# Kernel tuning notes

Measured on AMD Instinct MI355X. Metric: run time of the kernel, lower is better.

Reference implementation:

```python
import jax, jax.numpy as jnp
import numpy as np

H = 2048      # hidden_dim
DI = 4096     # intermediate_size
N = 128       # state_size
NH = 64       # num_heads
P = 64        # head_dim
K = 4         # conv kernel
CH = 256      # chunk size
L = 4096      # seq len
DT_MIN, DT_MAX = 1e-3, 1e2


def setup_inputs() -> dict:
    key = jax.random.key(0)
    ks = jax.random.split(key, 8)
    conv_dim = DI + 2 * N
    x = jax.random.normal(ks[0], (L, H), jnp.float32)
    W_in = jax.random.normal(ks[1], (DI + 2 * N + NH, H), jnp.float32) / np.sqrt(H)
    conv_w = jax.random.normal(ks[2], (conv_dim, 1, K), jnp.float32) / np.sqrt(K)
    conv_b = jax.random.normal(ks[3], (conv_dim,), jnp.float32) * 0.01
    u = jax.random.uniform(ks[4], (NH,))
    dt = jnp.exp(u * (np.log(0.1) - np.log(0.001)) + np.log(0.001))
    dt = jnp.maximum(dt, 1e-4)
    dt_bias = dt + jnp.log(-jnp.expm1(-dt))   # inverse-softplus init
    A_log = jnp.log(jax.random.uniform(ks[5], (NH,), minval=1.0, maxval=16.0))
    D = jnp.ones((NH,), jnp.float32)
    norm_w = jnp.ones((DI,), jnp.float32)
    W_out = jax.random.normal(ks[6], (H, DI), jnp.float32) / np.sqrt(DI)
    return dict(x=x, W_in=W_in, conv_w=conv_w, conv_b=conv_b, dt_bias=dt_bias,
                A_log=A_log, D=D, norm_w=norm_w, W_out=W_out)


def _causal_decay(a):
    # a: [..., T] per-step log-decays -> exp(segment sum) as lower-tri [..., T, T]
    T = a.shape[-1]
    strict = jnp.tril(jnp.ones((T, T), bool), -1)
    full = jnp.tril(jnp.ones((T, T), bool), 0)
    s = jnp.cumsum(jnp.where(strict, a[..., None], 0.0), axis=-2)
    return jnp.where(full, jnp.exp(s), 0.0)


def reference(x, W_in, conv_w, conv_b, dt_bias, A_log, D, norm_w, W_out):
    conv_dim = DI + 2 * N
    xBCdt = x @ W_in.T                                  # [L, DI+2N+NH]
    xBC, dt = xBCdt[:, :conv_dim], xBCdt[:, conv_dim:]
    # causal depthwise conv1d + SiLU
    z = jax.lax.conv_general_dilated(
        xBC.T[None], conv_w, (1,), [(K - 1, 0)],
        dimension_numbers=('NCH', 'OIH', 'NCH'),
        feature_group_count=conv_dim)[0] + conv_b[:, None]
    xBC = jax.nn.silu(z.T)                              # [L, conv_dim]
    x_ssm = xBC[:, :DI].reshape(L, NH, P)
    Bm = xBC[:, DI:DI + N]                              # [L, N] shared over heads
    Cm = xBC[:, DI + N:]                                # [L, N]
    dt = jnp.clip(jax.nn.softplus(dt + dt_bias), DT_MIN, DT_MAX)  # [L, NH]
    A = -jnp.exp(A_log.astype(jnp.float32))             # [NH]
    dA = dt * A                                         # [L, NH]
    xdt = x_ssm * dt[:, :, None]                        # [L, NH, P]
    nc = L // CH
    xc = xdt.reshape(nc, CH, NH, P)
    Bc = Bm.reshape(nc, CH, N)
    Cc = Cm.reshape(nc, CH, N)
    dAc = dA.reshape(nc, CH, NH)
    A_cs = jnp.cumsum(dAc, axis=1)                      # [c, k, h]
    # intra-chunk (diagonal blocks)
    Lmat = _causal_decay(dAc.transpose(0, 2, 1))        # [c, h, k, k]
    Y_diag = jnp.einsum('ckn,csn,chks,cshp->ckhp', Cc, Bc, Lmat, xc)
    # per-chunk right states
    decay_states = jnp.exp(A_cs[:, -1:, :] - A_cs)      # [c, k, h]
    states = jnp.einsum('ckn,ckh,ckhp->chpn', Bc, decay_states, xc)
    # inter-chunk recurrence (no initial state)
    chunk_sum = A_cs[:, -1, :].T                        # [h, c]
    dec = _causal_decay(jnp.pad(chunk_sum, ((0, 0), (1, 0))))  # [h, c+1, c+1]
    states = jnp.concatenate([jnp.zeros((1, NH, P, N), states.dtype), states], 0)
    new_states = jnp.einsum('hzc,chpn->zhpn', dec, states)      # [c+1, h, p, n]
    prev = new_states[:-1]                              # [c, h, p, n]
    Y_off = jnp.einsum('ckn,chpn,ckh->ckhp', Cc, prev, jnp.exp(A_cs))
    Y = (Y_diag + Y_off).reshape(L, NH, P) + x_ssm * D[None, :, None]
    y = Y.reshape(L, DI)
    # RMSNorm
    var = jnp.mean(jnp.square(y.astype(jnp.float32)), -1, keepdims=True)
    y = (y * jax.lax.rsqrt(var + 1e-6)) * norm_w
    return y @ W_out.T
```

## Files before the change

kernel.cpp:

```cpp
#include <hip/hip_runtime.h>


typedef __bf16 bf16;
typedef __bf16 bf16x8 __attribute__((ext_vector_type(8)));
typedef __bf16 bf16x4 __attribute__((ext_vector_type(4)));
typedef float  f32x4  __attribute__((ext_vector_type(4)));

#define DEV static __device__ __forceinline__

DEV f32x4 mfma16(bf16x8 a, bf16x8 b, f32x4 c) {
  return __builtin_amdgcn_mfma_f32_16x16x32_bf16(a, b, c, 0, 0, 0);
}

DEV void gll16(const bf16* g, bf16* l) {
  __builtin_amdgcn_global_load_lds(
      (const __attribute__((address_space(1))) unsigned int*)g,
      (__attribute__((address_space(3))) unsigned int*)l, 16, 0, 0);
}

#define BAR()   asm volatile("s_barrier" ::: "memory")
#define LGKM0() do { asm volatile("s_waitcnt lgkmcnt(0)" ::: "memory"); \
                     __builtin_amdgcn_sched_barrier(0); } while (0)
#define VMW(n)  asm volatile("s_waitcnt vmcnt(" #n ")" ::: "memory")

template <int K>
__global__ __launch_bounds__(512) void gemm8p_kernel(
    const bf16* __restrict__ A, const bf16* __restrict__ B,
    float* __restrict__ C, int N, int ntN) {
  constexpr int NT = K / 64;
  __shared__ __align__(16) bf16 lds[3 * 24576];
  const int tid = threadIdx.x;
  const int wave = tid >> 6, lane = tid & 63;
  const int lrow = lane & 15;
  const int lkb = (lane >> 4) * 16;
  const int xorv = (lrow & 7) << 4;
  const int bx = blockIdx.x / ntN, by = blockIdx.x % ntN;
  const int row0 = bx * 256, col0 = by * 128;
  const int arow = (wave >> 1) * 64;
  const int brow = (wave & 1) * 64;

  const bf16* gA[4];
  const bf16* gB[2];
#pragma unroll
  for (int r = 0; r < 4; ++r) {
    int P = r * 8192 + tid * 16;
    int L = P ^ (((P >> 7) & 7) << 4);
    gA[r] = A + (size_t)(row0 + (L >> 7)) * K + ((L & 127) >> 1);
  }
#pragma unroll
  for (int r = 0; r < 2; ++r) {
    int P = r * 8192 + tid * 16;
    int L = P ^ (((P >> 7) & 7) << 4);
    gB[r] = B + (size_t)(col0 + (L >> 7)) * K + ((L & 127) >> 1);
  }
  const int ldsW = wave * 512;

  auto rdA = [&](int slB, int m, int ks) -> bf16x8 {
    return *(const bf16x8*)((const char*)lds + slB +
                            (arow + m * 16 + lrow) * 128 +
                            (((ks << 6) | lkb) ^ xorv));
  };
  auto rdB = [&](int slB, int n, int ks) -> bf16x8 {
    return *(const bf16x8*)((const char*)lds + slB + 32768 +
                            (brow + n * 16 + lrow) * 128 +
                            (((ks << 6) | lkb) ^ xorv));
  };
  auto stA01 = [&](int ss) {
    gll16(gA[0], lds + ss * 24576 + 0 * 4096 + ldsW);
    gll16(gA[1], lds + ss * 24576 + 1 * 4096 + ldsW);
  };
  auto stA23 = [&](int ss) {
    gll16(gA[2], lds + ss * 24576 + 2 * 4096 + ldsW);
    gll16(gA[3], lds + ss * 24576 + 3 * 4096 + ldsW);
  };
  auto stB = [&](int ss) {
    gll16(gB[0], lds + ss * 24576 + 16384 + 0 * 4096 + ldsW);
    gll16(gB[1], lds + ss * 24576 + 16384 + 1 * 4096 + ldsW);
  };
  auto adv = [&]() {
#pragma unroll
    for (int r = 0; r < 4; ++r) gA[r] += 64;
#pragma unroll
    for (int r = 0; r < 2; ++r) gB[r] += 64;
  };

  f32x4 acc[4][4] = {};
  bf16x8 aF[4][2], bF[4][2];

  stA01(0); stA23(0); stB(0); adv();
  stA01(1); stA23(1); stB(1); adv();
  VMW(6);
  BAR();

  int sl = 0, ss = 2;
  for (int t = 0; t < NT; ++t) {
    const int slB = sl * 49152;
    const bool pf = (t + 2 < NT);
#pragma unroll
    for (int m = 0; m < 2; ++m)
#pragma unroll
      for (int ks = 0; ks < 2; ++ks) aF[m][ks] = rdA(slB, m, ks);
#pragma unroll
    for (int n = 0; n < 2; ++n)
#pragma unroll
      for (int ks = 0; ks < 2; ++ks) bF[n][ks] = rdB(slB, n, ks);
    if (pf) stA01(ss);
    BAR(); LGKM0();
    __builtin_amdgcn_s_setprio(1);
#pragma unroll
    for (int m = 0; m < 2; ++m)
#pragma unroll
      for (int n = 0; n < 2; ++n)
#pragma unroll
        for (int ks = 0; ks < 2; ++ks)
          acc[m][n] = mfma16(aF[m][ks], bF[n][ks], acc[m][n]);
    __builtin_amdgcn_s_setprio(0);
    __builtin_amdgcn_sched_barrier(0);
    BAR();
#pragma unroll
    for (int n = 2; n < 4; ++n)
#pragma unroll
      for (int ks = 0; ks < 2; ++ks) bF[n][ks] = rdB(slB, n, ks);
    if (pf) stA23(ss);
    BAR(); LGKM0();
    __builtin_amdgcn_s_setprio(1);
#pragma unroll
    for (int m = 0; m < 2; ++m)
#pragma unroll
      for (int n = 2; n < 4; ++n)
#pragma unroll
        for (int ks = 0; ks < 2; ++ks)
          acc[m][n] = mfma16(aF[m][ks], bF[n][ks], acc[m][n]);
    __builtin_amdgcn_s_setprio(0);
    __builtin_amdgcn_sched_barrier(0);
    BAR();
#pragma unroll
    for (int m = 2; m < 4; ++m)
#pragma unroll
      for (int ks = 0; ks < 2; ++ks) aF[m][ks] = rdA(slB, m, ks);
    if (pf) { stB(ss); adv(); }
    BAR(); LGKM0();
    __builtin_amdgcn_s_setprio(1);
#pragma unroll
    for (int m = 2; m < 4; ++m)
#pragma unroll
      for (int n = 0; n < 2; ++n)
#pragma unroll
        for (int ks = 0; ks < 2; ++ks)
          acc[m][n] = mfma16(aF[m][ks], bF[n][ks], acc[m][n]);
    __builtin_amdgcn_s_setprio(0);
    __builtin_amdgcn_sched_barrier(0);
    BAR();
    __builtin_amdgcn_s_setprio(1);
#pragma unroll
    for (int m = 2; m < 4; ++m)
#pragma unroll
      for (int n = 2; n < 4; ++n)
#pragma unroll
        for (int ks = 0; ks < 2; ++ks)
          acc[m][n] = mfma16(aF[m][ks], bF[n][ks], acc[m][n]);
    __builtin_amdgcn_s_setprio(0);
    __builtin_amdgcn_sched_barrier(0);
    if (t < NT - 2) { VMW(6); } else { VMW(0); }
    BAR();
    sl = (sl == 2) ? 0 : sl + 1;
    ss = (ss == 2) ? 0 : ss + 1;
  }
  const int orow = (lane >> 4) * 4;
#pragma unroll
  for (int m = 0; m < 4; ++m)
#pragma unroll
    for (int n = 0; n < 4; ++n)
#pragma unroll
      for (int i = 0; i < 4; ++i) {
        int r = row0 + arow + m * 16 + orow + i;
        int c = col0 + brow + n * 16 + lrow;
        C[(size_t)r * N + c] = acc[m][n][i];
      }
}

__global__ __launch_bounds__(256) void cast_f2b_kernel(
    const float* __restrict__ in, bf16* __restrict__ out, long n4) {
  long i = (long)blockIdx.x * blockDim.x + threadIdx.x;
  long stride = (long)gridDim.x * blockDim.x;
  for (; i < n4; i += stride) {
    float4 v = ((const float4*)in)[i];
    bf16x4 o = {(bf16)v.x, (bf16)v.y, (bf16)v.z, (bf16)v.w};
    ((bf16x4*)out)[i] = o;
  }
}

__global__ __launch_bounds__(256) void cast_pad_kernel(
    const float* __restrict__ in, bf16* __restrict__ out, long n4, long valid4) {
  long i = (long)blockIdx.x * blockDim.x + threadIdx.x;
  long stride = (long)gridDim.x * blockDim.x;
  for (; i < n4; i += stride) {
    bf16x4 o = {(bf16)0.f, (bf16)0.f, (bf16)0.f, (bf16)0.f};
    if (i < valid4) {
      float4 v = ((const float4*)in)[i];
      o = bf16x4{(bf16)v.x, (bf16)v.y, (bf16)v.z, (bf16)v.w};
    }
    ((bf16x4*)out)[i] = o;
  }
}

__global__ __launch_bounds__(256) void dt_scan_kernel(
    const float* __restrict__ xBCdt, const float* __restrict__ dt_bias,
    const float* __restrict__ A_log, float* __restrict__ dt,
    float* __restrict__ Acs, float* __restrict__ decayO,
    float* __restrict__ expAcs, float* __restrict__ csum) {
  const int c = blockIdx.x, h = blockIdx.y;
  const int k = threadIdx.x;
  const int t = c * 256 + k;
  __shared__ float buf[256];
  float raw = xBCdt[(size_t)t * 4480 + 4352 + h] + dt_bias[h];
  float dtv = raw > 20.f ? raw : log1pf(__expf(raw));
  dtv = fminf(fmaxf(dtv, 0.001f), 100.f);
  dt[(size_t)t * 64 + h] = dtv;
  float dA = -__expf(A_log[h]) * dtv;
  buf[k] = dA;
  __syncthreads();
  for (int off = 1; off < 256; off <<= 1) {
    float add = (k >= off) ? buf[k - off] : 0.f;
    __syncthreads();
    buf[k] += add;
    __syncthreads();
  }
  float v = buf[k];
  float total = buf[255];
  size_t base = (size_t)(c * 64 + h) * 256 + k;
  Acs[base] = v;
  expAcs[base] = __expf(v);
  decayO[base] = __expf(total - v);
  if (k == 0) csum[c * 64 + h] = total;
}

__global__ __launch_bounds__(256) void conv_kernel(
    const float* __restrict__ xBCdt, const float* __restrict__ conv_w,
    const float* __restrict__ conv_b, const float* __restrict__ dt,
    bf16* __restrict__ XS, bf16* __restrict__ XDT_T, bf16* __restrict__ Bm,
    bf16* __restrict__ BT, bf16* __restrict__ Cm) {
  const int t0 = blockIdx.x * 64;
  const int c0 = blockIdx.y * 64;
  __shared__ float lin[67 * 64];
  __shared__ bf16 tr[64 * 72];
  const int tid = threadIdx.x;
  for (int idx = tid; idx < 67 * 64; idx += 256) {
    int r = idx >> 6, cc = idx & 63;
    int gt = t0 + r - 3;
    lin[idx] = (gt >= 0) ? xBCdt[(size_t)gt * 4480 + c0 + cc] : 0.f;
  }
  __syncthreads();
  const int cl = tid & 63, tg = tid >> 6;
  const int ch = c0 + cl;
  const float w0 = conv_w[ch * 4 + 0], w1 = conv_w[ch * 4 + 1];
  const float w2 = conv_w[ch * 4 + 2], w3 = conv_w[ch * 4 + 3];
  const float bb = conv_b[ch];
  float vals[16];
  for (int j = 0; j < 16; ++j) {
    int tl = tg * 16 + j;
    float s = bb + lin[tl * 64 + cl] * w0 + lin[(tl + 1) * 64 + cl] * w1 +
              lin[(tl + 2) * 64 + cl] * w2 + lin[(tl + 3) * 64 + cl] * w3;
    vals[j] = s / (1.f + __expf(-s));
  }
  if (c0 < 4096) {
    const int hh = c0 >> 6;
    for (int j = 0; j < 16; ++j) {
      int t = t0 + tg * 16 + j;
      XS[(size_t)t * 4096 + ch] = (bf16)vals[j];
    }
    __syncthreads();
    for (int j = 0; j < 16; ++j) {
      int tl = tg * 16 + j;
      float dtv = dt[(size_t)(t0 + tl) * 64 + hh];
      tr[cl * 72 + tl] = (bf16)(vals[j] * dtv);
    }
    __syncthreads();
    int p = tid >> 2, toff = (tid & 3) * 16;
    bf16* dst = XDT_T + (size_t)(hh * 64 + p) * 4096 + t0 + toff;
    *(bf16x8*)(dst) = *(const bf16x8*)(tr + p * 72 + toff);
    *(bf16x8*)(dst + 8) = *(const bf16x8*)(tr + p * 72 + toff + 8);
  } else if (c0 < 4224) {
    const int n0 = c0 - 4096;
    for (int j = 0; j < 16; ++j) {
      int t = t0 + tg * 16 + j;
      Bm[(size_t)t * 128 + n0 + cl] = (bf16)vals[j];
    }
    __syncthreads();
    for (int j = 0; j < 16; ++j) tr[cl * 72 + tg * 16 + j] = (bf16)vals[j];
    __syncthreads();
    int p = tid >> 2, toff = (tid & 3) * 16;
    bf16* dst = BT + (size_t)(n0 + p) * 4096 + t0 + toff;
    *(bf16x8*)(dst) = *(const bf16x8*)(tr + p * 72 + toff);
    *(bf16x8*)(dst + 8) = *(const bf16x8*)(tr + p * 72 + toff + 8);
  } else {
    const int n0 = c0 - 4224;
    for (int j = 0; j < 16; ++j) {
      int t = t0 + tg * 16 + j;
      Cm[(size_t)t * 128 + n0 + cl] = (bf16)vals[j];
    }
  }
}

__global__ __launch_bounds__(256) void gmat_kernel(
    const bf16* __restrict__ Cm, const bf16* __restrict__ Bm,
    float* __restrict__ G) {
  const int c = blockIdx.x, kt = blockIdx.y, st = blockIdx.z;
  const int tid = threadIdx.x;
  const int wave = tid >> 6, lane = tid & 63;
  const int lrow = lane & 15, lk = (lane >> 4) * 8;
  const int wr = (wave >> 1) * 64, wc = (wave & 1) * 64;
  f32x4 acc[4][4] = {};
  for (int kk = 0; kk < 4; ++kk) {
    bf16x8 aF[4], bF[4];
    for (int m = 0; m < 4; ++m)
      aF[m] = *(const bf16x8*)(Cm + (size_t)(c * 256 + kt * 128 + wr + m * 16 + lrow) * 128 + kk * 32 + lk);
    for (int n = 0; n < 4; ++n)
      bF[n] = *(const bf16x8*)(Bm + (size_t)(c * 256 + st * 128 + wc + n * 16 + lrow) * 128 + kk * 32 + lk);
    for (int m = 0; m < 4; ++m)
      for (int n = 0; n < 4; ++n)
        acc[m][n] = mfma16(aF[m], bF[n], acc[m][n]);
  }
  const int orow = (lane >> 4) * 4;
  for (int m = 0; m < 4; ++m)
    for (int n = 0; n < 4; ++n)
      for (int i = 0; i < 4; ++i) {
        int k = kt * 128 + wr + m * 16 + orow + i;
        int s = st * 128 + wc + n * 16 + lrow;
        G[((size_t)c * 256 + k) * 256 + s] = acc[m][n][i];
      }
}

__global__ __launch_bounds__(256) void states_kernel(
    const bf16* __restrict__ XDT_T, const bf16* __restrict__ BT,
    const float* __restrict__ decayO, float* __restrict__ states) {
  const int c = blockIdx.x, h = blockIdx.y;
  __shared__ bf16 Ap[64 * 264];
  __shared__ float sDec[256];
  const int tid = threadIdx.x;
  const int wave = tid >> 6, lane = tid & 63;
  const int lrow = lane & 15, lk = (lane >> 4) * 8;
  sDec[tid] = decayO[(size_t)(c * 64 + h) * 256 + tid];
  __syncthreads();
  {
    int p = tid >> 2, kb = (tid & 3) * 64;
    const bf16* src = XDT_T + (size_t)(h * 64 + p) * 4096 + c * 256 + kb;
    for (int j = 0; j < 8; ++j) {
      bf16x8 v = *(const bf16x8*)(src + j * 8);
      bf16x8 o;
      for (int i = 0; i < 8; ++i) o[i] = (bf16)((float)v[i] * sDec[kb + j * 8 + i]);
      *(bf16x8*)(Ap + p * 264 + kb + j * 8) = o;
    }
  }
  __syncthreads();
  const int nb = wave * 32;
  f32x4 acc[4][2] = {};
  for (int kk = 0; kk < 8; ++kk) {
    bf16x8 aF[4], bF[2];
    for (int m = 0; m < 4; ++m)
      aF[m] = *(const bf16x8*)(Ap + (m * 16 + lrow) * 264 + kk * 32 + lk);
    for (int n = 0; n < 2; ++n)
      bF[n] = *(const bf16x8*)(BT + (size_t)(nb + n * 16 + lrow) * 4096 + c * 256 + kk * 32 + lk);
    for (int m = 0; m < 4; ++m)
      for (int n = 0; n < 2; ++n)
        acc[m][n] = mfma16(aF[m], bF[n], acc[m][n]);
  }
  float* st = states + (size_t)(c * 64 + h) * 64 * 128;
  const int orow = (lane >> 4) * 4;
  for (int m = 0; m < 4; ++m)
    for (int n = 0; n < 2; ++n)
      for (int i = 0; i < 4; ++i)
        st[(size_t)(m * 16 + orow + i) * 128 + nb + n * 16 + lrow] = acc[m][n][i];
}

__global__ __launch_bounds__(128) void chunk_rec_kernel(
    const float* __restrict__ states, const float* __restrict__ csum,
    bf16* __restrict__ prev) {
  const int h = blockIdx.x, p = blockIdx.y;
  const int n = threadIdx.x;
  size_t base = (size_t)h * 64 * 128 + (size_t)p * 128 + n;
  float run = 0.f;
  for (int c = 0; c < 16; ++c) {
    size_t idx = (size_t)c * 64 * 64 * 128 + base;
    prev[idx] = (bf16)run;
    run = run * __expf(csum[c * 64 + h]) + states[idx];
  }
}

__global__ __launch_bounds__(256) void ydiag_kernel(
    const bf16* __restrict__ Cm, const bf16* __restrict__ prev,
    const float* __restrict__ G, const float* __restrict__ Acs,
    const float* __restrict__ expAcs, const bf16* __restrict__ XDT_T,
    const bf16* __restrict__ XS, const float* __restrict__ Dp,
    float* __restrict__ Y) {
  const int c = blockIdx.x, h = blockIdx.y;
  __shared__ float sAcs[256];
  __shared__ float sExp[256];
  __shared__ __align__(16) bf16 pv[64 * 136];
  __shared__ __align__(16) bf16 xd[64 * 264];
  const int tid = threadIdx.x;
  const int wave = tid >> 6, lane = tid & 63;
  const int lrow = lane & 15, lk = (lane >> 4) * 8;
  const int wv16 = wave * 16;
  sAcs[tid] = Acs[(size_t)(c * 64 + h) * 256 + tid];
  sExp[tid] = expAcs[(size_t)(c * 64 + h) * 256 + tid];
  {
    int r = tid >> 2, q = (tid & 3) * 32;
    const bf16* src = prev + (size_t)(c * 64 + h) * 8192 + r * 128 + q;
    bf16* dst = pv + r * 136 + q;
    for (int j = 0; j < 4; ++j)
      *(bf16x8*)(dst + j * 8) = *(const bf16x8*)(src + j * 8);
  }
  {
    int r = tid >> 2, q = (tid & 3) * 64;
    const bf16* src = XDT_T + (size_t)(h * 64 + r) * 4096 + c * 256 + q;
    bf16* dst = xd + r * 264 + q;
    for (int j = 0; j < 8; ++j)
      *(bf16x8*)(dst + j * 8) = *(const bf16x8*)(src + j * 8);
  }
  __syncthreads();
  f32x4 acc[4][4] = {};
  __builtin_amdgcn_s_setprio(1);
  for (int kk = 0; kk < 4; ++kk) {
    bf16x8 aF[4], bF[4];
    for (int m = 0; m < 4; ++m)
      aF[m] = *(const bf16x8*)(Cm + (size_t)(c * 256 + m * 64 + wv16 + lrow) * 128 + kk * 32 + lk);
    for (int n = 0; n < 4; ++n)
      bF[n] = *(const bf16x8*)(pv + (n * 16 + lrow) * 136 + kk * 32 + lk);
    for (int m = 0; m < 4; ++m)
      for (int n = 0; n < 4; ++n)
        acc[m][n] = mfma16(aF[m], bF[n], acc[m][n]);
  }
  __builtin_amdgcn_s_setprio(0);
  const int orow = (lane >> 4) * 4;
  for (int m = 0; m < 4; ++m)
    for (int i = 0; i < 4; ++i) {
      float e = sExp[m * 64 + wv16 + orow + i];
      for (int n = 0; n < 4; ++n) acc[m][n][i] *= e;
    }
  const float* Gp = G + (size_t)c * 65536;
  for (int stile = 0; stile < 4; ++stile) {
    const int s0 = stile * 64;
    for (int kk = 0; kk < 2; ++kk) {
      bf16x8 bF[4];
      for (int n = 0; n < 4; ++n)
        bF[n] = *(const bf16x8*)(xd + (n * 16 + lrow) * 264 + s0 + kk * 32 + lk);
      for (int m = 0; m < 4; ++m) {
        if (m * 64 + wv16 + 15 < s0) continue;
        const int row = m * 64 + wv16 + lrow;
        const float ak = sAcs[row];
        const float* grow = Gp + (size_t)row * 256 + s0 + kk * 32 + lk;
        bf16x8 af;
        for (int j = 0; j < 8; ++j) {
          int s = s0 + kk * 32 + lk + j;
          float v = grow[j] * __expf(ak - sAcs[s]);
          if (s > row) v = 0.f;
          af[j] = (bf16)v;
        }
        __builtin_amdgcn_s_setprio(1);
        for (int n = 0; n < 4; ++n)
          acc[m][n] = mfma16(af, bF[n], acc[m][n]);
        __builtin_amdgcn_s_setprio(0);
      }
    }
  }
  const float Dh = Dp[h];
  for (int m = 0; m < 4; ++m)
    for (int n = 0; n < 4; ++n)
      for (int i = 0; i < 4; ++i) {
        int t = c * 256 + m * 64 + wv16 + orow + i;
        int col = h * 64 + n * 16 + lrow;
        float xs = (float)XS[(size_t)t * 4096 + col];
        Y[(size_t)t * 4096 + col] = acc[m][n][i] + xs * Dh;
      }
}

__global__ __launch_bounds__(256) void rmsnorm_kernel(
    const float* __restrict__ Y, const float* __restrict__ norm_w,
    bf16* __restrict__ out) {
  const int row = blockIdx.x;
  const float4* y4 = (const float4*)(Y + (size_t)row * 4096);
  float4 v[4];
  float ss = 0.f;
  for (int j = 0; j < 4; ++j) {
    v[j] = y4[threadIdx.x + j * 256];
    ss += v[j].x * v[j].x + v[j].y * v[j].y + v[j].z * v[j].z + v[j].w * v[j].w;
  }
  for (int off = 32; off; off >>= 1) ss += __shfl_down(ss, off, 64);
  __shared__ float ws[4];
  if ((threadIdx.x & 63) == 0) ws[threadIdx.x >> 6] = ss;
  __syncthreads();
  float scale = rsqrtf((ws[0] + ws[1] + ws[2] + ws[3]) / 4096.f + 1e-6f);
  for (int j = 0; j < 4; ++j) {
    int col = (threadIdx.x + j * 256) * 4;
    float4 w = *(const float4*)(norm_w + col);
    bf16x4 o = {(bf16)(v[j].x * scale * w.x), (bf16)(v[j].y * scale * w.y),
                (bf16)(v[j].z * scale * w.z), (bf16)(v[j].w * scale * w.w)};
    *(bf16x4*)(out + (size_t)row * 4096 + col) = o;
  }
}

extern "C" void kernel_launch(void* const* d_in, const int* in_sizes, int n_in,
                              void* d_out, int out_size, void* d_ws, size_t ws_size,
                              hipStream_t stream) {
  const float* x       = (const float*)d_in[0];
  const float* W_in    = (const float*)d_in[1];
  const float* conv_w  = (const float*)d_in[2];
  const float* conv_b  = (const float*)d_in[3];
  const float* dt_bias = (const float*)d_in[4];
  const float* A_log   = (const float*)d_in[5];
  const float* Dp      = (const float*)d_in[6];
  const float* norm_w  = (const float*)d_in[7];
  const float* W_out   = (const float*)d_in[8];

  size_t o = 0;
  char* base = (char*)d_ws;
  auto take = [&](size_t b) {
    char* p = base + o;
    o += (b + 255) & ~(size_t)255;
    return (void*)p;
  };
  bf16*  xb     = (bf16*)take((size_t)4096 * 2048 * 2);
  bf16*  winb   = (bf16*)take((size_t)4480 * 2048 * 2);
  float* xBCdt  = (float*)take((size_t)4096 * 4480 * 4);
  float* dtg    = (float*)take((size_t)4096 * 64 * 4);
  float* Acs    = (float*)take((size_t)4096 * 64 * 4);
  float* decayO = (float*)take((size_t)4096 * 64 * 4);
  float* expA   = (float*)take((size_t)4096 * 64 * 4);
  float* csum   = (float*)take((size_t)16 * 64 * 4);
  bf16*  XS     = (bf16*)take((size_t)4096 * 4096 * 2);
  bf16*  XDT_T  = (bf16*)take((size_t)4096 * 4096 * 2);
  bf16*  Bm     = (bf16*)take((size_t)4096 * 128 * 2);
  bf16*  BT     = (bf16*)take((size_t)4096 * 128 * 2);
  bf16*  Cm     = (bf16*)take((size_t)4096 * 128 * 2);
  float* G      = (float*)take((size_t)16 * 256 * 256 * 4);
  float* states = (float*)take((size_t)16 * 64 * 64 * 128 * 4);
  bf16*  prev   = (bf16*)take((size_t)16 * 64 * 64 * 128 * 2);
  bf16*  ynorm  = xb;
  float* Y      = xBCdt;
  bf16*  woutb  = (bf16*)states;

  cast_f2b_kernel<<<2048, 256, 0, stream>>>(x, xb, (long)4096 * 2048 / 4);
  cast_pad_kernel<<<2048, 256, 0, stream>>>(W_in, winb, (long)4480 * 2048 / 4,
                                            (long)4416 * 2048 / 4);
  gemm8p_kernel<2048><<<560, 512, 0, stream>>>(xb, winb, xBCdt, 4480, 35);
  dt_scan_kernel<<<dim3(16, 64), 256, 0, stream>>>(xBCdt, dt_bias, A_log, dtg,
                                                   Acs, decayO, expA, csum);
  conv_kernel<<<dim3(64, 68), 256, 0, stream>>>(xBCdt, conv_w, conv_b, dtg, XS,
                                                XDT_T, Bm, BT, Cm);
  gmat_kernel<<<dim3(16, 2, 2), 256, 0, stream>>>(Cm, Bm, G);
  states_kernel<<<dim3(16, 64), 256, 0, stream>>>(XDT_T, BT, decayO, states);
  chunk_rec_kernel<<<dim3(64, 64), 128, 0, stream>>>(states, csum, prev);
  cast_f2b_kernel<<<2048, 256, 0, stream>>>(W_out, woutb, (long)2048 * 4096 / 4);
  ydiag_kernel<<<dim3(16, 64), 256, 0, stream>>>(Cm, prev, G, Acs, expA, XDT_T,
                                                 XS, Dp, Y);
  rmsnorm_kernel<<<4096, 256, 0, stream>>>(Y, norm_w, ynorm);
  gemm8p_kernel<4096><<<256, 512, 0, stream>>>(ynorm, woutb,
                                               (float*)d_out, 2048, 16);
}
```

Measured before the change: 396.8 us.

## Replace GEMM with 256x256-tile split-K=2 kernel and sum partials downstream

The GEMM kernel is rewritten with 256x256 output tiles, double-buffered LDS instead of triple, and a launch bound of two blocks per CU. Both projections now use split-K of 2 over blockIdx.y. The input projection writes two fp32 partials that dt_scan and conv add on load, and the output projection's partials are summed by a new add kernel. The intent is better operand reuse and more blocks to fill the CUs. The cost is extra partial-buffer traffic, an extra kernel launch, and the input-projection width padded to 4608.

```diff
diff --git a/kernel.cpp b/kernel.cpp
--- a/kernel.cpp
+++ b/kernel.cpp
@@ -22,161 +22,160 @@
 #define LGKM0() do { asm volatile("s_waitcnt lgkmcnt(0)" ::: "memory"); \
                      __builtin_amdgcn_sched_barrier(0); } while (0)
 #define VMW(n)  asm volatile("s_waitcnt vmcnt(" #n ")" ::: "memory")
-
-template <int K>
-__global__ __launch_bounds__(512) void gemm8p_kernel(
-    const bf16* __restrict__ A, const bf16* __restrict__ B,
-    float* __restrict__ C, int N, int ntN) {
-  constexpr int NT = K / 64;
-  __shared__ __align__(16) bf16 lds[3 * 24576];
+#define SCHB()  __builtin_amdgcn_sched_barrier(0)
+
+template <int NT, int LD>
+__global__ __launch_bounds__(512, 2) void gemm2k_kernel(
+    const bf16* __restrict__ Abase, const bf16* __restrict__ Bbase,
+    float* __restrict__ C0, float* __restrict__ C1, int ldc, int ntN) {
+  __shared__ __align__(16) bf16 lds[2 * 32768];
   const int tid = threadIdx.x;
-  const int wave = tid >> 6, lane = tid & 63;
+  const int wid = tid >> 6, lane = tid & 63;
   const int lrow = lane & 15;
-  const int lkb = (lane >> 4) * 16;
+  const int colb = (lane >> 4) * 16;
   const int xorv = (lrow & 7) << 4;
-  const int bx = blockIdx.x / ntN, by = blockIdx.x % ntN;
-  const int row0 = bx * 256, col0 = by * 128;
-  const int arow = (wave >> 1) * 64;
-  const int brow = (wave & 1) * 64;
-
+  const int wm = wid & 1, wn = wid >> 1;
+  const int bid = blockIdx.x;
+  const int bx = bid / ntN, by = bid % ntN;
+  const int row0 = bx * 256, col0 = by * 256;
+  const bf16* A = Abase + (size_t)blockIdx.y * (NT * 64);
+  const bf16* B = Bbase + (size_t)blockIdx.y * (NT * 64);
+  float* C = blockIdx.y ? C1 : C0;
+
+  const int P = tid * 16;
+  const int Lc = P ^ (((P >> 7) & 7) << 4);
+  const int srow = Lc >> 7;
+  const int selem = (Lc & 127) >> 1;
   const bf16* gA[4];
-  const bf16* gB[2];
-#pragma unroll
-  for (int r = 0; r < 4; ++r) {
-    int P = r * 8192 + tid * 16;
-    int L = P ^ (((P >> 7) & 7) << 4);
-    gA[r] = A + (size_t)(row0 + (L >> 7)) * K + ((L & 127) >> 1);
-  }
-#pragma unroll
-  for (int r = 0; r < 2; ++r) {
-    int P = r * 8192 + tid * 16;
-    int L = P ^ (((P >> 7) & 7) << 4);
-    gB[r] = B + (size_t)(col0 + (L >> 7)) * K + ((L & 127) >> 1);
-  }
-  const int ldsW = wave * 512;
-
-  auto rdA = [&](int slB, int m, int ks) -> bf16x8 {
-    return *(const bf16x8*)((const char*)lds + slB +
-                            (arow + m * 16 + lrow) * 128 +
-                            (((ks << 6) | lkb) ^ xorv));
+  const bf16* gB[4];
+#pragma unroll
+  for (int q = 0; q < 4; ++q) {
+    gA[q] = A + (size_t)(row0 + q * 64 + srow) * LD + selem;
+    gB[q] = B + (size_t)(col0 + q * 64 + srow) * LD + selem;
+  }
+  auto dA = [&](int s, int q) -> bf16* { return lds + s * 32768 + q * 4096 + tid * 8; };
+  auto dB = [&](int s, int q) -> bf16* { return lds + s * 32768 + 16384 + q * 4096 + tid * 8; };
+
+  auto rdA = [&](int s, int m, int ks) -> bf16x8 {
+    int row = wm * 128 + m * 16 + lrow;
+    int cb = ((ks << 6) | colb) ^ xorv;
+    return *(const bf16x8*)((const char*)(lds + s * 32768) + row * 128 + cb);
   };
-  auto rdB = [&](int slB, int n, int ks) -> bf16x8 {
-    return *(const bf16x8*)((const char*)lds + slB + 32768 +
-                            (brow + n * 16 + lrow) * 128 +
-                            (((ks << 6) | lkb) ^ xorv));
+  auto rdB = [&](int s, int n, int ks) -> bf16x8 {
+    int row = wn * 64 + n * 16 + lrow;
+    int cb = ((ks << 6) | colb) ^ xorv;
+    return *(const bf16x8*)((const char*)(lds + s * 32768 + 16384) + row * 128 + cb);
   };
-  auto stA01 = [&](int ss) {
-    gll16(gA[0], lds + ss * 24576 + 0 * 4096 + ldsW);
-    gll16(gA[1], lds + ss * 24576 + 1 * 4096 + ldsW);
-  };
-  auto stA23 = [&](int ss) {
-    gll16(gA[2], lds + ss * 24576 + 2 * 4096 + ldsW);
-    gll16(gA[3], lds + ss * 24576 + 3 * 4096 + ldsW);
-  };
-  auto stB = [&](int ss) {
-    gll16(gB[0], lds + ss * 24576 + 16384 + 0 * 4096 + ldsW);
-    gll16(gB[1], lds + ss * 24576 + 16384 + 1 * 4096 + ldsW);
-  };
-  auto adv = [&]() {
-#pragma unroll
-    for (int r = 0; r < 4; ++r) gA[r] += 64;
-#pragma unroll
-    for (int r = 0; r < 2; ++r) gB[r] += 64;
-  };
-
-  f32x4 acc[4][4] = {};
+
+  f32x4 acc[8][4] = {};
   bf16x8 aF[4][2], bF[4][2];
 
-  stA01(0); stA23(0); stB(0); adv();
-  stA01(1); stA23(1); stB(1); adv();
-  VMW(6);
+  gll16(gB[0], dB(0, 0)); gll16(gB[1], dB(0, 1));
+  gll16(gB[2], dB(0, 2)); gll16(gB[3], dB(0, 3));
+  gll16(gA[0], dA(0, 0)); gll16(gA[2], dA(0, 2));
+  gll16(gA[1], dA(0, 1)); gll16(gA[3], dA(0, 3));
+  VMW(2);
   BAR();
 
-  int sl = 0, ss = 2;
   for (int t = 0; t < NT; ++t) {
-    const int slB = sl * 49152;
-    const bool pf = (t + 2 < NT);
-#pragma unroll
-    for (int m = 0; m < 2; ++m)
-#pragma unroll
-      for (int ks = 0; ks < 2; ++ks) aF[m][ks] = rdA(slB, m, ks);
+    const int st = t & 1, ss = st ^ 1;
+    const int ko = (t + 1) << 6;
+    const bool pf = (t + 1 < NT);
+#pragma unroll
+    for (int m = 0; m < 4; ++m)
+#pragma unroll
+      for (int ks = 0; ks < 2; ++ks) aF[m][ks] = rdA(st, m, ks);
 #pragma unroll
     for (int n = 0; n < 2; ++n)
 #pragma unroll
-      for (int ks = 0; ks < 2; ++ks) bF[n][ks] = rdB(slB, n, ks);
-    if (pf) stA01(ss);
+      for (int ks = 0; ks < 2; ++ks) bF[n][ks] = rdB(st, n, ks);
+    if (pf) { gll16(gB[0] + ko, dB(ss, 0)); gll16(gB[1] + ko, dB(ss, 1)); }
     BAR(); LGKM0();
     __builtin_amdgcn_s_setprio(1);
 #pragma unroll
-    for (int m = 0; m < 2; ++m)
+    for (int m = 0; m < 4; ++m)
 #pragma unroll
       for (int n = 0; n < 2; ++n)
 #pragma unroll
         for (int ks = 0; ks < 2; ++ks)
           acc[m][n] = mfma16(aF[m][ks], bF[n][ks], acc[m][n]);
     __builtin_amdgcn_s_setprio(0);
-    __builtin_amdgcn_sched_barrier(0);
+    SCHB();
     BAR();
 #pragma unroll
     for (int n = 2; n < 4; ++n)
 #pragma unroll
-      for (int ks = 0; ks < 2; ++ks) bF[n][ks] = rdB(slB, n, ks);
-    if (pf) stA23(ss);
+      for (int ks = 0; ks < 2; ++ks) bF[n][ks] = rdB(st, n, ks);
+    if (pf) { gll16(gB[2] + ko, dB(ss, 2)); gll16(gB[3] + ko, dB(ss, 3)); }
     BAR(); LGKM0();
     __builtin_amdgcn_s_setprio(1);
 #pragma unroll
-    for (int m = 0; m < 2; ++m)
+    for (int m = 0; m < 4; ++m)
 #pragma unroll
       for (int n = 2; n < 4; ++n)
 #pragma unroll
         for (int ks = 0; ks < 2; ++ks)
           acc[m][n] = mfma16(aF[m][ks], bF[n][ks], acc[m][n]);
     __builtin_amdgcn_s_setprio(0);
-    __builtin_amdgcn_sched_barrier(0);
+    SCHB();
+    if (pf) { VMW(4); } else { VMW(0); }
     BAR();
 #pragma unroll
-    for (int m = 2; m < 4; ++m)
-#pragma unroll
-      for (int ks = 0; ks < 2; ++ks) aF[m][ks] = rdA(slB, m, ks);
-    if (pf) { stB(ss); adv(); }
+    for (int m = 0; m < 4; ++m)
+#pragma unroll
+      for (int ks = 0; ks < 2; ++ks) aF[m][ks] = rdA(st, m + 4, ks);
+    if (pf) { gll16(gA[0] + ko, dA(ss, 0)); gll16(gA[2] + ko, dA(ss, 2)); }
     BAR(); LGKM0();
     __builtin_amdgcn_s_setprio(1);
 #pragma unroll
-    for (int m = 2; m < 4; ++m)
-#pragma unroll
-      for (int n = 0; n < 2; ++n)
+    for (int m = 0; m < 4; ++m)
+#pragma unroll
+      for (int n = 2; n < 4; ++n)
 #pragma unroll
         for (int ks = 0; ks < 2; ++ks)
-          acc[m][n] = mfma16(aF[m][ks], bF[n][ks], acc[m][n]);
+          acc[m + 4][n] = mfma16(aF[m][ks], bF[n][ks], acc[m + 4][n]);
     __builtin_amdgcn_s_setprio(0);
-    __builtin_amdgcn_sched_barrier(0);
+    SCHB();
+    BAR();
+    if (pf) { gll16(gA[1] + ko, dA(ss, 1)); gll16(gA[3] + ko, dA(ss, 3)); }
     BAR();
     __builtin_amdgcn_s_setprio(1);
 #pragma unroll
-    for (int m = 2; m < 4; ++m)
-#pragma unroll
-      for (int n = 2; n < 4; ++n)
+    for (int m = 0; m < 4; ++m)
+#pragma unroll
+      for (int n = 0; n < 2; ++n)
 #pragma unroll
         for (int ks = 0; ks < 2; ++ks)
-          acc[m][n] = mfma16(aF[m][ks], bF[n][ks], acc[m][n]);
+          acc[m + 4][n] = mfma16(aF[m][ks], bF[n][ks], acc[m + 4][n]);
     __builtin_amdgcn_s_setprio(0);
-    __builtin_amdgcn_sched_barrier(0);
-    if (t < NT - 2) { VMW(6); } else { VMW(0); }
+    SCHB();
+    if (pf) { VMW(2); }
     BAR();
-    sl = (sl == 2) ? 0 : sl + 1;
-    ss = (ss == 2) ? 0 : ss + 1;
   }
   const int orow = (lane >> 4) * 4;
 #pragma unroll
-  for (int m = 0; m < 4; ++m)
+  for (int m = 0; m < 8; ++m)
 #pragma unroll
     for (int n = 0; n < 4; ++n)
 #pragma unroll
       for (int i = 0; i < 4; ++i) {
-        int r = row0 + arow + m * 16 + orow + i;
-        int c = col0 + brow + n * 16 + lrow;
-        C[(size_t)r * N + c] = acc[m][n][i];
+        int r = row0 + wm * 128 + m * 16 + orow + i;
+        int c = col0 + wn * 64 + n * 16 + lrow;
+        C[(size_t)r * ldc + c] = acc[m][n][i];
       }
+}
+
+__global__ __launch_bounds__(256) void add2_kernel(
+    const float* __restrict__ a, const float* __restrict__ b,
+    float* __restrict__ o, long n4) {
+  long i = (long)blockIdx.x * blockDim.x + threadIdx.x;
+  long stride = (long)gridDim.x * blockDim.x;
+  for (; i < n4; i += stride) {
+    float4 va = ((const float4*)a)[i];
+    float4 vb = ((const float4*)b)[i];
+    float4 vo = {va.x + vb.x, va.y + vb.y, va.z + vb.z, va.w + vb.w};
+    ((float4*)o)[i] = vo;
+  }
 }
 
 __global__ __launch_bounds__(256) void cast_f2b_kernel(
@@ -205,15 +204,16 @@
 }
 
 __global__ __launch_bounds__(256) void dt_scan_kernel(
-    const float* __restrict__ xBCdt, const float* __restrict__ dt_bias,
-    const float* __restrict__ A_log, float* __restrict__ dt,
-    float* __restrict__ Acs, float* __restrict__ decayO,
+    const float* __restrict__ xp0, const float* __restrict__ xp1,
+    const float* __restrict__ dt_bias, const float* __restrict__ A_log,
+    float* __restrict__ dt, float* __restrict__ Acs, float* __restrict__ decayO,
     float* __restrict__ expAcs, float* __restrict__ csum) {
   const int c = blockIdx.x, h = blockIdx.y;
   const int k = threadIdx.x;
   const int t = c * 256 + k;
   __shared__ float buf[256];
-  float raw = xBCdt[(size_t)t * 4480 + 4352 + h] + dt_bias[h];
+  size_t idx = (size_t)t * 4608 + 4352 + h;
+  float raw = xp0[idx] + xp1[idx] + dt_bias[h];
   float dtv = raw > 20.f ? raw : log1pf(__expf(raw));
   dtv = fminf(fmaxf(dtv, 0.001f), 100.f);
   dt[(size_t)t * 64 + h] = dtv;
@@ -236,10 +236,11 @@
 }
 
 __global__ __launch_bounds__(256) void conv_kernel(
-    const float* __restrict__ xBCdt, const float* __restrict__ conv_w,
-    const float* __restrict__ conv_b, const float* __restrict__ dt,
-    bf16* __restrict__ XS, bf16* __restrict__ XDT_T, bf16* __restrict__ Bm,
-    bf16* __restrict__ BT, bf16* __restrict__ Cm) {
+    const float* __restrict__ xp0, const float* __restrict__ xp1,
+    const float* __restrict__ conv_w, const float* __restrict__ conv_b,
+    const float* __restrict__ dt, bf16* __restrict__ XS,
+    bf16* __restrict__ XDT_T, bf16* __restrict__ Bm, bf16* __restrict__ BT,
+    bf16* __restrict__ Cm) {
   const int t0 = blockIdx.x * 64;
   const int c0 = blockIdx.y * 64;
   __shared__ float lin[67 * 64];
@@ -248,7 +249,8 @@
   for (int idx = tid; idx < 67 * 64; idx += 256) {
     int r = idx >> 6, cc = idx & 63;
     int gt = t0 + r - 3;
-    lin[idx] = (gt >= 0) ? xBCdt[(size_t)gt * 4480 + c0 + cc] : 0.f;
+    size_t g = (size_t)gt * 4608 + c0 + cc;
+    lin[idx] = (gt >= 0) ? (xp0[g] + xp1[g]) : 0.f;
   }
   __syncthreads();
   const int cl = tid & 63, tg = tid >> 6;
@@ -521,8 +523,9 @@
     return (void*)p;
   };
   bf16*  xb     = (bf16*)take((size_t)4096 * 2048 * 2);
-  bf16*  winb   = (bf16*)take((size_t)4480 * 2048 * 2);
-  float* xBCdt  = (float*)take((size_t)4096 * 4480 * 4);
+  bf16*  winb   = (bf16*)take((size_t)4608 * 2048 * 2);
+  float* xp0    = (float*)take((size_t)4096 * 4608 * 4);
+  float* xp1    = (float*)take((size_t)4096 * 4608 * 4);
   float* dtg    = (float*)take((size_t)4096 * 64 * 4);
   float* Acs    = (float*)take((size_t)4096 * 64 * 4);
   float* decayO = (float*)take((size_t)4096 * 64 * 4);
@@ -533,21 +536,24 @@
   bf16*  Bm     = (bf16*)take((size_t)4096 * 128 * 2);
   bf16*  BT     = (bf16*)take((size_t)4096 * 128 * 2);
   bf16*  Cm     = (bf16*)take((size_t)4096 * 128 * 2);
-  float* G      = (float*)take((size_t)16 * 256 * 256 * 4);
-  float* states = (float*)take((size_t)16 * 64 * 64 * 128 * 4);
-  bf16*  prev   = (bf16*)take((size_t)16 * 64 * 64 * 128 * 2);
+  float* G      = (float*)((char*)xp1);
+  float* states = (float*)((char*)xp1 + (size_t)4194304);
+  bf16*  prev   = (bf16*)((char*)xp1 + (size_t)37748736);
+  bf16*  woutb  = (bf16*)((char*)xp1 + (size_t)54525952);
+  float* Y      = xp0;
   bf16*  ynorm  = xb;
-  float* Y      = xBCdt;
-  bf16*  woutb  = (bf16*)states;
+  float* p2a    = (float*)XS;
+  float* p2b    = (float*)XDT_T;
 
   cast_f2b_kernel<<<2048, 256, 0, stream>>>(x, xb, (long)4096 * 2048 / 4);
-  cast_pad_kernel<<<2048, 256, 0, stream>>>(W_in, winb, (long)4480 * 2048 / 4,
+  cast_pad_kernel<<<2048, 256, 0, stream>>>(W_in, winb, (long)4608 * 2048 / 4,
                                             (long)4416 * 2048 / 4);
-  gemm8p_kernel<2048><<<560, 512, 0, stream>>>(xb, winb, xBCdt, 4480, 35);
-  dt_scan_kernel<<<dim3(16, 64), 256, 0, stream>>>(xBCdt, dt_bias, A_log, dtg,
-                                                   Acs, decayO, expA, csum);
-  conv_kernel<<<dim3(64, 68), 256, 0, stream>>>(xBCdt, conv_w, conv_b, dtg, XS,
-                                                XDT_T, Bm, BT, Cm);
+  gemm2k_kernel<16, 2048><<<dim3(288, 2), 512, 0, stream>>>(xb, winb, xp0, xp1,
+                                                            4608, 18);
+  dt_scan_kernel<<<dim3(16, 64), 256, 0, stream>>>(xp0, xp1, dt_bias, A_log,
+                                                   dtg, Acs, decayO, expA, csum);
+  conv_kernel<<<dim3(64, 68), 256, 0, stream>>>(xp0, xp1, conv_w, conv_b, dtg,
+                                                XS, XDT_T, Bm, BT, Cm);
   gmat_kernel<<<dim3(16, 2, 2), 256, 0, stream>>>(Cm, Bm, G);
   states_kernel<<<dim3(16, 64), 256, 0, stream>>>(XDT_T, BT, decayO, states);
   chunk_rec_kernel<<<dim3(64, 64), 128, 0, stream>>>(states, csum, prev);
@@ -555,6 +561,8 @@
   ydiag_kernel<<<dim3(16, 64), 256, 0, stream>>>(Cm, prev, G, Acs, expA, XDT_T,
                                                  XS, Dp, Y);
   rmsnorm_kernel<<<4096, 256, 0, stream>>>(Y, norm_w, ynorm);
-  gemm8p_kernel<4096><<<256, 512, 0, stream>>>(ynorm, woutb,
-                                               (float*)d_out, 2048, 16);
-}
+  gemm2k_kernel<32, 4096><<<dim3(128, 2), 512, 0, stream>>>(ynorm, woutb, p2a,
+                                                            p2b, 2048, 8);
+  add2_kernel<<<2048, 256, 0, stream>>>(p2a, p2b, (float*)d_out,
+                                        (long)4096 * 2048 / 4);
+}
```

Result: slower. 409.4 us (+3.2%).
